# Kernel optimization log

Hardware: AMD Instinct MI355X
Metric: run time of the kernel (lower is better)

The kernel has to match this reference:

```python
import jax, jax.numpy as jnp
import numpy as np

IN_FEATURES = 4096
OUT_FEATURES = 11008
GROUP_SIZE = 128
NUM_GROUPS = IN_FEATURES // GROUP_SIZE  # 32
BATCH, SEQ = 4, 2048


def setup_inputs() -> dict:
    key = jax.random.key(0)
    k_in, k_w, k_s, k_b = jax.random.split(key, 4)
    inp = jax.random.normal(k_in, (BATCH, SEQ, IN_FEATURES), dtype=jnp.float32)
    # 4-bit symmetric codes in [-8, 8)
    weight = jax.random.randint(k_w, (OUT_FEATURES, NUM_GROUPS, GROUP_SIZE), -8, 8, dtype=jnp.int32)
    # small positive per-group scales, as produced by quantization calibration
    scales = jax.random.uniform(k_s, (OUT_FEATURES, NUM_GROUPS), dtype=jnp.float32) * 0.02 + 1e-4
    bias = jax.random.normal(k_b, (OUT_FEATURES,), dtype=jnp.float32)
    return {"input": inp, "weight": weight, "scales": scales, "bias": bias}


def reference(input, weight, scales, bias):
    # Fused dequant-matmul: symmetric weight-only quantization.
    # weight: [O, G, gs] int codes; scales: [O, G] per-group scale.
    O, G, gs = weight.shape
    W = weight.astype(jnp.float32) * scales[:, :, None]   # [O, G, gs] dequantized
    W = W.reshape(O, G * gs)                               # [O, in_features]
    out = jnp.einsum('bsi,oi->bso', input, W)              # [B, S, O]
    return out + bias
```

## Files before the change

kernel.cpp:

```cpp
#include <hip/hip_runtime.h>
#include <hip/hip_bf16.h>
#include <cstdint>

#define M_DIM 8192
#define K_DIM 4096
#define N_DIM 11008
#define NGROUPS 32

typedef __attribute__((ext_vector_type(4))) float f32x4;
typedef __attribute__((ext_vector_type(4))) int i32x4;
typedef __attribute__((ext_vector_type(8))) __bf16 bf16x8;

__device__ __forceinline__ unsigned int f2bf(float f) {
  unsigned int u = __builtin_bit_cast(unsigned int, f);
  return (u + 0x7FFFu + ((u >> 16) & 1u)) >> 16;
}
__device__ __forceinline__ unsigned int pk2(float lo, float hi) {
  return f2bf(lo) | (f2bf(hi) << 16);
}

__global__ __launch_bounds__(256) void quantA_kernel(const float* __restrict__ in,
                                                     char* __restrict__ outA,
                                                     float* __restrict__ sA) {
  const int row = blockIdx.x * 4 + (threadIdx.x >> 6);
  const int lane = threadIdx.x & 63;
  const f32x4* p4 = (const f32x4*)(in + (size_t)row * K_DIM);
  f32x4 v[16];
#pragma unroll
  for (int e = 0; e < 16; ++e)
    v[e] = __builtin_nontemporal_load(&p4[e * 64 + lane]);
  float mx = 0.f;
#pragma unroll
  for (int e = 0; e < 16; ++e)
    mx = fmaxf(mx, fmaxf(fmaxf(fabsf(v[e].x), fabsf(v[e].y)),
                         fmaxf(fabsf(v[e].z), fabsf(v[e].w))));
#pragma unroll
  for (int off = 32; off; off >>= 1) mx = fmaxf(mx, __shfl_xor(mx, off));
  mx = fmaxf(mx, 1e-30f);
  const float rq = 127.f / mx;
  if (lane == 0) sA[row] = mx / 127.f;
  char* op = outA + (size_t)row * K_DIM;
#pragma unroll
  for (int e = 0; e < 16; ++e) {
    unsigned pk = ((unsigned)((int)rintf(v[e].x * rq)) & 0xFFu)
                | (((unsigned)((int)rintf(v[e].y * rq)) & 0xFFu) << 8)
                | (((unsigned)((int)rintf(v[e].z * rq)) & 0xFFu) << 16)
                | (((unsigned)((int)rintf(v[e].w * rq)) & 0xFFu) << 24);
    *(unsigned*)(op + e * 256 + lane * 4) = pk;
  }
}

__global__ __launch_bounds__(256) void quantW_kernel(const int* __restrict__ wc,
                                                     const float* __restrict__ sc,
                                                     char* __restrict__ outB,
                                                     float* __restrict__ sW) {
  const int col = blockIdx.x * 4 + (threadIdx.x >> 6);
  const int lane = threadIdx.x & 63;
  const i32x4* p = (const i32x4*)(wc + (size_t)col * K_DIM);
  const float* scp = sc + col * NGROUPS;
  i32x4 c[16];
  float s[16];
#pragma unroll
  for (int e = 0; e < 16; ++e) {
    c[e] = __builtin_nontemporal_load(&p[e * 64 + lane]);
    s[e] = scp[e * 2 + (lane >> 5)];
  }
  float mx = 0.f;
#pragma unroll
  for (int e = 0; e < 16; ++e) {
    float m = fmaxf(fmaxf(fabsf((float)c[e].x), fabsf((float)c[e].y)),
                    fmaxf(fabsf((float)c[e].z), fabsf((float)c[e].w)));
    mx = fmaxf(mx, m * s[e]);
  }
#pragma unroll
  for (int off = 32; off; off >>= 1) mx = fmaxf(mx, __shfl_xor(mx, off));
  mx = fmaxf(mx, 1e-30f);
  const float rq = 127.f / mx;
  if (lane == 0) sW[col] = mx / 127.f;
  char* op = outB + (size_t)col * K_DIM;
#pragma unroll
  for (int e = 0; e < 16; ++e) {
    const float sq = s[e] * rq;
    unsigned pk = ((unsigned)((int)rintf((float)c[e].x * sq)) & 0xFFu)
                | (((unsigned)((int)rintf((float)c[e].y * sq)) & 0xFFu) << 8)
                | (((unsigned)((int)rintf((float)c[e].z * sq)) & 0xFFu) << 16)
                | (((unsigned)((int)rintf((float)c[e].w * sq)) & 0xFFu) << 24);
    *(unsigned*)(op + e * 256 + lane * 4) = pk;
  }
}

__device__ __forceinline__ void gload16(const void* g, void* l) {
  __builtin_amdgcn_global_load_lds((const __attribute__((address_space(1))) void*)g,
                                   (__attribute__((address_space(3))) void*)l,
                                   16, 0, 0);
}

#define BM 256
#define BN 128
#define BKB 64
#define NKT (K_DIM / BKB)
#define TILES_M (M_DIM / BM)
#define TILES_N (N_DIM / BN)
#define NB2 (TILES_M * TILES_N)
#define TSZA (BM * BKB)
#define TSZB (BN * BKB)

#define VMCNT_(n) asm volatile("s_waitcnt vmcnt(" #n ")" ::: "memory")
#define VMCNT(n) VMCNT_(n)
#define BAR() __builtin_amdgcn_s_barrier()

__global__ __launch_bounds__(512, 4) void gemmq_kernel(
    const char* __restrict__ A,
    const char* __restrict__ B,
    const float* __restrict__ sA,
    const float* __restrict__ sW,
    const float* __restrict__ bias,
    float* __restrict__ out) {
  __shared__ __align__(16) char lA[3][TSZA];
  __shared__ __align__(16) char lB[3][TSZB];

  const int t = threadIdx.x;
  const int bid = blockIdx.x;
  const int wg = (bid & 7) * (NB2 / 8) + (bid >> 3);
  const int m0 = (wg / TILES_N) * BM;
  const int n0 = (wg % TILES_N) * BN;

  const int w = t >> 6;
  const int lane = t & 63;
  const int wm = w >> 1;
  const int wn = w & 1;

  const int ra0 = w * 32 + (lane >> 2);
  const int ra1 = ra0 + 16;
  const int rb = w * 16 + (lane >> 2);
  const int pgs = lane & 3;
  const size_t aoff0 = (size_t)(m0 + ra0) * K_DIM + (unsigned)(pgs ^ ((ra0 >> 1) & 3)) * 16;
  const size_t aoff1 = (size_t)(m0 + ra1) * K_DIM + (unsigned)(pgs ^ ((ra1 >> 1) & 3)) * 16;
  const size_t boff = (size_t)(n0 + rb) * K_DIM + (unsigned)(pgs ^ ((rb >> 1) & 3)) * 16;
  const int ldA0 = w * 2048;
  const int ldA1 = w * 2048 + 1024;
  const int ldB = w * 1024;

  i32x4 acc[4][4];
#pragma unroll
  for (int i = 0; i < 4; ++i)
#pragma unroll
    for (int j = 0; j < 4; ++j) {
      i32x4 z = {0, 0, 0, 0};
      acc[i][j] = z;
    }

#define STAGE(buf, kt)                                                        \
  do {                                                                        \
    gload16(A + aoff0 + (size_t)(kt) * BKB, &lA[buf][ldA0]);                  \
    gload16(A + aoff1 + (size_t)(kt) * BKB, &lA[buf][ldA1]);                  \
    gload16(B + boff + (size_t)(kt) * BKB, &lB[buf][ldB]);                    \
  } while (0)

#define TILE_CORE(CB)                                                         \
  i32x4 af[4], bq[4];                                                         \
  _Pragma("unroll") for (int i = 0; i < 4; ++i) {                             \
    const int row = wm * 64 + i * 16 + (lane & 15);                           \
    const int pg = (lane >> 4) ^ ((row >> 1) & 3);                            \
    af[i] = *(const i32x4*)&lA[CB][row * 64 + pg * 16];                       \
  }                                                                           \
  _Pragma("unroll") for (int j = 0; j < 4; ++j) {                             \
    const int row = wn * 64 + j * 16 + (lane & 15);                           \
    const int pg = (lane >> 4) ^ ((row >> 1) & 3);                            \
    bq[j] = *(const i32x4*)&lB[CB][row * 64 + pg * 16];                       \
  }

#define TILE_MMA()                                                            \
  __builtin_amdgcn_s_setprio(1);                                              \
  _Pragma("unroll") for (int i = 0; i < 4; ++i)                               \
  _Pragma("unroll") for (int j = 0; j < 4; ++j)                               \
    acc[i][j] = __builtin_amdgcn_mfma_i32_16x16x64_i8(af[i], bq[j],           \
                                                      acc[i][j], 0, 0, 0);    \
  __builtin_amdgcn_s_setprio(0);

#define TILE(CB, SB, KT2)                                                     \
  {                                                                           \
    TILE_CORE(CB)                                                             \
    STAGE(SB, KT2);                                                           \
    TILE_MMA()                                                                \
    VMCNT(3);                                                                 \
    BAR();                                                                    \
  }

  STAGE(0, 0);
  STAGE(1, 1);
  VMCNT(3);
  BAR();

  for (int it = 0; it < 20; ++it) {
    const int k = 3 * it;
    TILE(0, 2, k + 2)
    TILE(1, 0, k + 3)
    TILE(2, 1, k + 4)
  }
  TILE(0, 2, 62)
  TILE(1, 0, 63)
  {
    TILE_CORE(2)
    TILE_MMA()
    VMCNT(0);
    BAR();
  }
  {
    TILE_CORE(0)
    TILE_MMA()
  }

  const int colb = n0 + wn * 64 + (lane & 15);
  const int rowb = m0 + wm * 64 + ((lane >> 4) << 2);
  float sar[4][4];
#pragma unroll
  for (int ai = 0; ai < 4; ++ai)
#pragma unroll
    for (int r = 0; r < 4; ++r)
      sar[ai][r] = sA[rowb + ai * 16 + r];
#pragma unroll
  for (int j = 0; j < 4; ++j) {
    const int col = colb + j * 16;
    const float sc2 = sW[col];
    const float bv = bias[col];
#pragma unroll
    for (int ai = 0; ai < 4; ++ai) {
      const int row = rowb + ai * 16;
#pragma unroll
      for (int r = 0; r < 4; ++r) {
        const float vout = (float)acc[ai][j][r] * sar[ai][r] * sc2 + bv;
        __builtin_nontemporal_store(vout, &out[(size_t)(row + r) * N_DIM + col]);
      }
    }
  }
#undef STAGE
#undef TILE_CORE
#undef TILE_MMA
#undef TILE
}

#define FBM 128
#define FBN 128
#define FBK 64
#define FNT_N 86
#define FNT_M 64
#define FNB (FNT_N * FNT_M)

__global__ __launch_bounds__(256, 2) void gemm_fb_kernel(
    const float* __restrict__ Ain, const int* __restrict__ Wcodes,
    const float* __restrict__ scales, const float* __restrict__ bias,
    float* __restrict__ out) {
  __shared__ unsigned short lsA[FBM * FBK];
  __shared__ unsigned short lsB[FBN * FBK];

  const int t = threadIdx.x;
  const int bid = blockIdx.x;
  const int wg = (bid & 7) * (FNB / 8) + (bid >> 3);
  const int m0 = (wg / FNT_N) * FBM;
  const int n0 = (wg % FNT_N) * FBN;

  const int w = t >> 6;
  const int lane = t & 63;
  const int wm = w >> 1, wn = w & 1;
  const int srow = t >> 3;
  const int sp = t & 7;
  const int skc = sp ^ (srow & 7);

  f32x4 acc[4][4];
#pragma unroll
  for (int i = 0; i < 4; ++i)
#pragma unroll
    for (int j = 0; j < 4; ++j) {
      f32x4 z = {0.f, 0.f, 0.f, 0.f};
      acc[i][j] = z;
    }

  for (int kt = 0; kt < K_DIM / FBK; ++kt) {
    const int kg = kt * FBK + skc * 8;
#pragma unroll
    for (int c = 0; c < 4; ++c) {
      const int arow = m0 + c * 32 + srow;
      const float* ap = Ain + (size_t)arow * K_DIM + kg;
      float4 a0 = *(const float4*)ap;
      float4 a1 = *(const float4*)(ap + 4);
      uint4 va;
      va.x = pk2(a0.x, a0.y); va.y = pk2(a0.z, a0.w);
      va.z = pk2(a1.x, a1.y); va.w = pk2(a1.z, a1.w);
      *(uint4*)&lsA[(c * 32 + srow) * FBK + sp * 8] = va;

      const int nrow = n0 + c * 32 + srow;
      const float s = scales[nrow * NGROUPS + (kg >> 7)];
      const int4* wp = (const int4*)(Wcodes + (size_t)nrow * K_DIM + kg);
      int4 c0 = wp[0], c1 = wp[1];
      uint4 vb;
      vb.x = pk2((float)c0.x * s, (float)c0.y * s);
      vb.y = pk2((float)c0.z * s, (float)c0.w * s);
      vb.z = pk2((float)c1.x * s, (float)c1.y * s);
      vb.w = pk2((float)c1.z * s, (float)c1.w * s);
      *(uint4*)&lsB[(c * 32 + srow) * FBK + sp * 8] = vb;
    }
    __syncthreads();
#pragma unroll
    for (int kk = 0; kk < 2; ++kk) {
      bf16x8 af[4], bfr[4];
#pragma unroll
      for (int i = 0; i < 4; ++i) {
        const int row = wm * 64 + i * 16 + (lane & 15);
        const int pg = (kk * 4 + (lane >> 4)) ^ (row & 7);
        af[i] = *(const bf16x8*)&lsA[row * FBK + pg * 8];
      }
#pragma unroll
      for (int j = 0; j < 4; ++j) {
        const int row = wn * 64 + j * 16 + (lane & 15);
        const int pg = (kk * 4 + (lane >> 4)) ^ (row & 7);
        bfr[j] = *(const bf16x8*)&lsB[row * FBK + pg * 8];
      }
#pragma unroll
      for (int i = 0; i < 4; ++i)
#pragma unroll
        for (int j = 0; j < 4; ++j)
          acc[i][j] = __builtin_amdgcn_mfma_f32_16x16x32_bf16(af[i], bfr[j], acc[i][j], 0, 0, 0);
    }
    __syncthreads();
  }

  const int colb = n0 + wn * 64 + (lane & 15);
  const int rowb = m0 + wm * 64 + ((lane >> 4) << 2);
#pragma unroll
  for (int j = 0; j < 4; ++j) {
    const int col = colb + j * 16;
    const float bv = bias[col];
#pragma unroll
    for (int i = 0; i < 4; ++i) {
      const int row = rowb + i * 16;
#pragma unroll
      for (int r = 0; r < 4; ++r)
        out[(size_t)(row + r) * N_DIM + col] = acc[i][j][r] + bv;
    }
  }
}

extern "C" void kernel_launch(void* const* d_in, const int* in_sizes, int n_in,
                              void* d_out, int out_size, void* d_ws, size_t ws_size,
                              hipStream_t stream) {
  const float* Ain = (const float*)d_in[0];
  const int* Wc = (const int*)d_in[1];
  const float* sc = (const float*)d_in[2];
  const float* bias = (const float*)d_in[3];
  float* out = (float*)d_out;

  const size_t offW = (size_t)M_DIM * K_DIM;
  const size_t offSA = offW + (size_t)N_DIM * K_DIM;
  const size_t offSW = offSA + (size_t)M_DIM * 4;
  const size_t need = offSW + (size_t)N_DIM * 4;

  if (ws_size >= need) {
    char* wsA = (char*)d_ws;
    char* wsB = (char*)d_ws + offW;
    float* sA = (float*)((char*)d_ws + offSA);
    float* sW = (float*)((char*)d_ws + offSW);
    quantA_kernel<<<M_DIM / 4, 256, 0, stream>>>(Ain, wsA, sA);
    quantW_kernel<<<N_DIM / 4, 256, 0, stream>>>(Wc, sc, wsB, sW);
    gemmq_kernel<<<NB2, 512, 0, stream>>>(wsA, wsB, sA, sW, bias, out);
  } else {
    gemm_fb_kernel<<<FNB, 256, 0, stream>>>(Ain, Wc, sc, bias, out);
  }
}
```

Measured before the change: 470.3 us.

## Switch int8 GEMM to 32x32x32 MFMA with fragment-ordered LDS layout

Replaces the 16x16x64 int8 MFMA tiling (4x4 accumulators per wave) with 32x32x32 int8 MFMA (2x2 accumulators, two k-substeps). Global-to-LDS staging now writes data in the exact per-lane fragment order, so LDS reads become contiguous lane*16 loads and the XOR swizzle is dropped. The epilogue is remapped to the 32x32 accumulator row layout. The goal is fewer MFMA issues and simpler LDS addressing, at the risk of changed LDS bank behaviour and longer per-instruction latency.

```diff
diff --git a/kernel.cpp b/kernel.cpp
--- a/kernel.cpp
+++ b/kernel.cpp
@@ -9,6 +9,7 @@
 
 typedef __attribute__((ext_vector_type(4))) float f32x4;
 typedef __attribute__((ext_vector_type(4))) int i32x4;
+typedef __attribute__((ext_vector_type(16))) int i32x16;
 typedef __attribute__((ext_vector_type(8))) __bf16 bf16x8;
 
 __device__ __forceinline__ unsigned int f2bf(float f) {
@@ -129,52 +130,45 @@
   const int lane = t & 63;
   const int wm = w >> 1;
   const int wn = w & 1;
-
-  const int ra0 = w * 32 + (lane >> 2);
-  const int ra1 = ra0 + 16;
-  const int rb = w * 16 + (lane >> 2);
-  const int pgs = lane & 3;
-  const size_t aoff0 = (size_t)(m0 + ra0) * K_DIM + (unsigned)(pgs ^ ((ra0 >> 1) & 3)) * 16;
-  const size_t aoff1 = (size_t)(m0 + ra1) * K_DIM + (unsigned)(pgs ^ ((ra1 >> 1) & 3)) * 16;
-  const size_t boff = (size_t)(n0 + rb) * K_DIM + (unsigned)(pgs ^ ((rb >> 1) & 3)) * 16;
+  const int l31 = lane & 31;
+  const int l5 = lane >> 5;
+
+  const size_t aoff = (size_t)(m0 + w * 32 + l31) * K_DIM + (unsigned)(l5 * 16);
+  const size_t boff = (size_t)(n0 + (w >> 1) * 32 + l31) * K_DIM
+                    + (unsigned)((w & 1) * 32 + l5 * 16);
   const int ldA0 = w * 2048;
   const int ldA1 = w * 2048 + 1024;
   const int ldB = w * 1024;
 
-  i32x4 acc[4][4];
-#pragma unroll
-  for (int i = 0; i < 4; ++i)
-#pragma unroll
-    for (int j = 0; j < 4; ++j) {
-      i32x4 z = {0, 0, 0, 0};
-      acc[i][j] = z;
-    }
+  i32x16 acc[2][2];
+#pragma unroll
+  for (int i = 0; i < 2; ++i)
+#pragma unroll
+    for (int j = 0; j < 2; ++j)
+      acc[i][j] = (i32x16)(0);
 
 #define STAGE(buf, kt)                                                        \
   do {                                                                        \
-    gload16(A + aoff0 + (size_t)(kt) * BKB, &lA[buf][ldA0]);                  \
-    gload16(A + aoff1 + (size_t)(kt) * BKB, &lA[buf][ldA1]);                  \
+    gload16(A + aoff + (size_t)(kt) * BKB, &lA[buf][ldA0]);                   \
+    gload16(A + aoff + (size_t)(kt) * BKB + 32, &lA[buf][ldA1]);              \
     gload16(B + boff + (size_t)(kt) * BKB, &lB[buf][ldB]);                    \
   } while (0)
 
 #define TILE_CORE(CB)                                                         \
-  i32x4 af[4], bq[4];                                                         \
-  _Pragma("unroll") for (int i = 0; i < 4; ++i) {                             \
-    const int row = wm * 64 + i * 16 + (lane & 15);                           \
-    const int pg = (lane >> 4) ^ ((row >> 1) & 3);                            \
-    af[i] = *(const i32x4*)&lA[CB][row * 64 + pg * 16];                       \
-  }                                                                           \
-  _Pragma("unroll") for (int j = 0; j < 4; ++j) {                             \
-    const int row = wn * 64 + j * 16 + (lane & 15);                           \
-    const int pg = (lane >> 4) ^ ((row >> 1) & 3);                            \
-    bq[j] = *(const i32x4*)&lB[CB][row * 64 + pg * 16];                       \
-  }
+  i32x4 af[2][2], bq[2][2];                                                   \
+  _Pragma("unroll") for (int i = 0; i < 2; ++i)                               \
+  _Pragma("unroll") for (int ks = 0; ks < 2; ++ks)                            \
+    af[i][ks] = *(const i32x4*)&lA[CB][(2 * wm + i) * 2048 + ks * 1024 + lane * 16]; \
+  _Pragma("unroll") for (int j = 0; j < 2; ++j)                               \
+  _Pragma("unroll") for (int ks = 0; ks < 2; ++ks)                            \
+    bq[j][ks] = *(const i32x4*)&lB[CB][((2 * wn + j) * 2 + ks) * 1024 + lane * 16];
 
 #define TILE_MMA()                                                            \
   __builtin_amdgcn_s_setprio(1);                                              \
-  _Pragma("unroll") for (int i = 0; i < 4; ++i)                               \
-  _Pragma("unroll") for (int j = 0; j < 4; ++j)                               \
-    acc[i][j] = __builtin_amdgcn_mfma_i32_16x16x64_i8(af[i], bq[j],           \
+  _Pragma("unroll") for (int ks = 0; ks < 2; ++ks)                            \
+  _Pragma("unroll") for (int i = 0; i < 2; ++i)                               \
+  _Pragma("unroll") for (int j = 0; j < 2; ++j)                               \
+    acc[i][j] = __builtin_amdgcn_mfma_i32_32x32x32_i8(af[i][ks], bq[j][ks],   \
                                                       acc[i][j], 0, 0, 0);    \
   __builtin_amdgcn_s_setprio(0);
 
@@ -211,26 +205,27 @@
     TILE_MMA()
   }
 
-  const int colb = n0 + wn * 64 + (lane & 15);
-  const int rowb = m0 + wm * 64 + ((lane >> 4) << 2);
-  float sar[4][4];
-#pragma unroll
-  for (int ai = 0; ai < 4; ++ai)
-#pragma unroll
-    for (int r = 0; r < 4; ++r)
-      sar[ai][r] = sA[rowb + ai * 16 + r];
-#pragma unroll
-  for (int j = 0; j < 4; ++j) {
-    const int col = colb + j * 16;
+  const int colb = n0 + wn * 64 + (lane & 31);
+  const int rowb = m0 + wm * 64 + ((lane >> 5) << 2);
+  float sar[2][16];
+#pragma unroll
+  for (int i = 0; i < 2; ++i)
+#pragma unroll
+    for (int r = 0; r < 16; ++r)
+      sar[i][r] = sA[rowb + i * 32 + (r & 3) + 8 * (r >> 2)];
+#pragma unroll
+  for (int j = 0; j < 2; ++j) {
+    const int col = colb + j * 32;
     const float sc2 = sW[col];
     const float bv = bias[col];
 #pragma unroll
-    for (int ai = 0; ai < 4; ++ai) {
-      const int row = rowb + ai * 16;
-#pragma unroll
-      for (int r = 0; r < 4; ++r) {
-        const float vout = (float)acc[ai][j][r] * sar[ai][r] * sc2 + bv;
-        __builtin_nontemporal_store(vout, &out[(size_t)(row + r) * N_DIM + col]);
+    for (int i = 0; i < 2; ++i) {
+      const int rowf = rowb + i * 32;
+#pragma unroll
+      for (int r = 0; r < 16; ++r) {
+        const int row = rowf + (r & 3) + 8 * (r >> 2);
+        const float vout = (float)acc[i][j][r] * sar[i][r] * sc2 + bv;
+        __builtin_nontemporal_store(vout, &out[(size_t)row * N_DIM + col]);
       }
     }
   }
```

Result: slower. 640.7 us (+36.2%).
